# Kernel tuning notes

Measured on AMD Instinct MI355X. Metric: run time of the kernel, lower is better.

## Reference

```python
import jax, jax.numpy as jnp
import numpy as np

DIM = 256
BATCH = 131072


def setup_inputs() -> dict:
    key = jax.random.key(0)
    kx, kl, ku = jax.random.split(key, 3)
    x = jax.random.normal(kx, (BATCH, DIM), dtype=jnp.float32)
    # l: unit lower-triangular (eye + strict lower random), as in __init__
    l = jnp.eye(DIM, dtype=jnp.float32) + jnp.tril(
        jax.random.normal(kl, (DIM, DIM), dtype=jnp.float32), -1)
    # u: unit upper-triangular (eye + strict upper random)
    u = jnp.eye(DIM, dtype=jnp.float32) + jnp.triu(
        jax.random.normal(ku, (DIM, DIM), dtype=jnp.float32), 1)
    # p: fixed random permutation matrix (buffer, not trained)
    perm = np.random.RandomState(0).permutation(DIM)
    p = jnp.zeros((DIM, DIM), dtype=jnp.float32).at[
        np.arange(DIM), perm].set(1.0)
    return {"x": x, "p": p, "l": l, "u": u}


def reference(x, p, l, u):
    # forward (reverse=False): w = p @ l @ u ; y = (w @ x.T).T = x @ w.T
    w = p @ l @ u                      # [dim, dim]
    y = x @ w.T                        # [batch, dim]
    # log|det(w)| = log|det(u)| since p is a permutation (|det|=1) and l is
    # unit-triangular; u is upper-triangular so det(u) = prod(diag(u)).
    log_det = jnp.sum(jnp.log(jnp.abs(jnp.diag(u))))
    return (y, log_det)
```

## Files before the change

### kernel.cpp

```cpp
#include <hip/hip_runtime.h>

#define DIM 256
#define BATCH 131072

#define BM 128
#define BN 256
#define BK 32
#define STRIDE 40

typedef __attribute__((ext_vector_type(8))) short s16x8;
typedef __attribute__((ext_vector_type(8))) unsigned short u16x8;
typedef __attribute__((ext_vector_type(4))) float f32x4;

static __device__ __forceinline__ unsigned short f2bf(float f) {
    unsigned int u = __builtin_bit_cast(unsigned int, f);
    u = (u + 0x7FFFu + ((u >> 16) & 1u)) >> 16;
    return (unsigned short)u;
}

__global__ void lu_mm(const float* __restrict__ l, const float* __restrict__ u,
                      float* __restrict__ m) {
    __shared__ float sL[DIM];
    const int i = blockIdx.x, j = threadIdx.x;
    sL[j] = l[i * DIM + j];
    __syncthreads();
    float s0 = 0.f, s1 = 0.f, s2 = 0.f, s3 = 0.f;
    #pragma unroll 4
    for (int k = 0; k < DIM; k += 4) {
        s0 = fmaf(sL[k + 0], u[(k + 0) * DIM + j], s0);
        s1 = fmaf(sL[k + 1], u[(k + 1) * DIM + j], s1);
        s2 = fmaf(sL[k + 2], u[(k + 2) * DIM + j], s2);
        s3 = fmaf(sL[k + 3], u[(k + 3) * DIM + j], s3);
    }
    m[i * DIM + j] = (s0 + s1) + (s2 + s3);
}

__global__ void perm_conv(const float* __restrict__ p, const float* __restrict__ m,
                          unsigned short* __restrict__ wbt) {
    __shared__ int srcRow;
    const int i = blockIdx.x, j = threadIdx.x;
    if (p[i * DIM + j] != 0.0f) srcRow = j;
    __syncthreads();
    wbt[i * DIM + j] = f2bf(m[srcRow * DIM + j]);
}

__global__ void logdet_kernel(const float* __restrict__ u, float* __restrict__ out) {
    const int i = threadIdx.x;
    float v = logf(fabsf(u[i * DIM + i]));
    #pragma unroll
    for (int o = 32; o; o >>= 1) v += __shfl_down(v, o, 64);
    __shared__ float partial[4];
    if ((i & 63) == 0) partial[i >> 6] = v;
    __syncthreads();
    if (i == 0) out[0] = (partial[0] + partial[1]) + (partial[2] + partial[3]);
}

__global__ __launch_bounds__(512) void gemm_xwT(const float* __restrict__ x,
                                                const unsigned short* __restrict__ wbt,
                                                float* __restrict__ y) {
    __shared__ unsigned short sA[BM * STRIDE];
    __shared__ unsigned short sB[BN * STRIDE];

    const int t    = threadIdx.x;
    const int lane = t & 63;
    const int wid  = t >> 6;
    const int wr   = wid >> 2;
    const int wc   = wid & 3;
    const int row0 = blockIdx.x * BM;

    const int ar = t >> 2;
    const int ac = (t & 3) * 4;
    const int br = t >> 1;
    const int bc = (t & 1) * 16;

    const int lr = lane & 15;
    const int lg = lane >> 4;

    f32x4 acc[4][4];
    #pragma unroll
    for (int m = 0; m < 4; m++)
        #pragma unroll
        for (int n = 0; n < 4; n++) acc[m][n] = (f32x4){0.f, 0.f, 0.f, 0.f};

    for (int ks = 0; ks < DIM / BK; ++ks) {
        const int k0 = ks * BK;
        if (ks) __syncthreads();
        {
            const float* src = x + (size_t)(row0 + ar) * DIM + k0 + ac;
            const float4 v0 = *(const float4*)(src);
            const float4 v1 = *(const float4*)(src + 16);
            ushort4 h0 = { f2bf(v0.x), f2bf(v0.y), f2bf(v0.z), f2bf(v0.w) };
            ushort4 h1 = { f2bf(v1.x), f2bf(v1.y), f2bf(v1.z), f2bf(v1.w) };
            *(ushort4*)&sA[ar * STRIDE + ac]      = h0;
            *(ushort4*)&sA[ar * STRIDE + ac + 16] = h1;
        }
        {
            const unsigned short* src = wbt + br * DIM + k0 + bc;
            const u16x8 w0 = *(const u16x8*)(src);
            const u16x8 w1 = *(const u16x8*)(src + 8);
            *(u16x8*)&sB[br * STRIDE + bc]     = w0;
            *(u16x8*)&sB[br * STRIDE + bc + 8] = w1;
        }
        __syncthreads();

        s16x8 af[4], bfr[4];
        #pragma unroll
        for (int m = 0; m < 4; m++)
            af[m] = *(const s16x8*)&sA[(wr * 64 + m * 16 + lr) * STRIDE + lg * 8];
        #pragma unroll
        for (int n = 0; n < 4; n++)
            bfr[n] = *(const s16x8*)&sB[(wc * 64 + n * 16 + lr) * STRIDE + lg * 8];
        #pragma unroll
        for (int m = 0; m < 4; m++)
            #pragma unroll
            for (int n = 0; n < 4; n++)
                acc[m][n] = __builtin_amdgcn_mfma_f32_16x16x32_bf16(af[m], bfr[n], acc[m][n], 0, 0, 0);
    }

    #pragma unroll
    for (int m = 0; m < 4; m++) {
        const int gr0 = row0 + wr * 64 + m * 16 + lg * 4;
        #pragma unroll
        for (int n = 0; n < 4; n++) {
            const int gc = wc * 64 + n * 16 + lr;
            #pragma unroll
            for (int j = 0; j < 4; j++)
                y[(size_t)(gr0 + j) * DIM + gc] = acc[m][n][j];
        }
    }
}

extern "C" void kernel_launch(void* const* d_in, const int* in_sizes, int n_in,
                              void* d_out, int out_size, void* d_ws, size_t ws_size,
                              hipStream_t stream) {
    const float* x = (const float*)d_in[0];
    const float* p = (const float*)d_in[1];
    const float* l = (const float*)d_in[2];
    const float* u = (const float*)d_in[3];
    float* out = (float*)d_out;

    float* mtmp = (float*)d_ws;
    unsigned short* wbt = (unsigned short*)((char*)d_ws + DIM * DIM * 4);

    lu_mm<<<DIM, DIM, 0, stream>>>(l, u, mtmp);
    perm_conv<<<DIM, DIM, 0, stream>>>(p, mtmp, wbt);
    logdet_kernel<<<1, DIM, 0, stream>>>(u, out + (size_t)BATCH * DIM);
    gemm_xwT<<<BATCH / BM, 512, 0, stream>>>(x, wbt, out);
}
```

Baseline: 68.39 us.

## Drop LDS staging in GEMM, load MFMA fragments from global; fuse LU and permute

The GEMM no longer stages tiles in shared memory. Each wave loads its A fragments straight from global x, converting them to bf16 in registers, and its B fragments straight from the bf16 weight, with no __syncthreads. The block tile shrinks to 64 rows with launch bounds (512,4), which should raise occupancy. Separately, the L·U product and the permutation/bf16 conversion are fused into one kernel that scatters rows to their permuted destinations. This saves one launch and the intermediate buffer. The risks are less coalesced global access and redundant W reads per wave, which lean on the cache.

```diff
diff --git a/kernel.cpp b/kernel.cpp
--- a/kernel.cpp
+++ b/kernel.cpp
@@ -2,11 +2,8 @@
 
 #define DIM 256
 #define BATCH 131072
-
-#define BM 128
-#define BN 256
-#define BK 32
-#define STRIDE 40
+#define BM 64
+#define NT 8
 
 typedef __attribute__((ext_vector_type(8))) short s16x8;
 typedef __attribute__((ext_vector_type(8))) unsigned short u16x8;
@@ -18,11 +15,13 @@
     return (unsigned short)u;
 }
 
-__global__ void lu_mm(const float* __restrict__ l, const float* __restrict__ u,
-                      float* __restrict__ m) {
+__global__ void lu_perm(const float* __restrict__ l, const float* __restrict__ u,
+                        const float* __restrict__ p, unsigned short* __restrict__ wbt) {
     __shared__ float sL[DIM];
+    __shared__ int dest;
     const int i = blockIdx.x, j = threadIdx.x;
     sL[j] = l[i * DIM + j];
+    if (p[j * DIM + i] != 0.0f) dest = j;
     __syncthreads();
     float s0 = 0.f, s1 = 0.f, s2 = 0.f, s3 = 0.f;
     #pragma unroll 4
@@ -32,16 +31,7 @@
         s2 = fmaf(sL[k + 2], u[(k + 2) * DIM + j], s2);
         s3 = fmaf(sL[k + 3], u[(k + 3) * DIM + j], s3);
     }
-    m[i * DIM + j] = (s0 + s1) + (s2 + s3);
-}
-
-__global__ void perm_conv(const float* __restrict__ p, const float* __restrict__ m,
-                          unsigned short* __restrict__ wbt) {
-    __shared__ int srcRow;
-    const int i = blockIdx.x, j = threadIdx.x;
-    if (p[i * DIM + j] != 0.0f) srcRow = j;
-    __syncthreads();
-    wbt[i * DIM + j] = f2bf(m[srcRow * DIM + j]);
+    wbt[dest * DIM + j] = f2bf((s0 + s1) + (s2 + s3));
 }
 
 __global__ void logdet_kernel(const float* __restrict__ u, float* __restrict__ out) {
@@ -55,77 +45,63 @@
     if (i == 0) out[0] = (partial[0] + partial[1]) + (partial[2] + partial[3]);
 }
 
-__global__ __launch_bounds__(512) void gemm_xwT(const float* __restrict__ x,
-                                                const unsigned short* __restrict__ wbt,
-                                                float* __restrict__ y) {
-    __shared__ unsigned short sA[BM * STRIDE];
-    __shared__ unsigned short sB[BN * STRIDE];
-
+__global__ __launch_bounds__(512, 4) void gemm_xwT(const float* __restrict__ x,
+                                                   const unsigned short* __restrict__ wbt,
+                                                   float* __restrict__ y) {
     const int t    = threadIdx.x;
     const int lane = t & 63;
     const int wid  = t >> 6;
     const int wr   = wid >> 2;
     const int wc   = wid & 3;
-    const int row0 = blockIdx.x * BM;
+    const int lr   = lane & 15;
+    const int lg   = lane >> 4;
+    const long row0 = (long)blockIdx.x * BM;
 
-    const int ar = t >> 2;
-    const int ac = (t & 3) * 4;
-    const int br = t >> 1;
-    const int bc = (t & 1) * 16;
+    const float*          xa = x   + (row0 + wr * 32 + lr) * DIM + lg * 8;
+    const unsigned short* bb = wbt + (wc * 64 + lr) * DIM + lg * 8;
 
-    const int lr = lane & 15;
-    const int lg = lane >> 4;
-
-    f32x4 acc[4][4];
+    f32x4 acc[2][4];
     #pragma unroll
-    for (int m = 0; m < 4; m++)
+    for (int m = 0; m < 2; m++)
         #pragma unroll
         for (int n = 0; n < 4; n++) acc[m][n] = (f32x4){0.f, 0.f, 0.f, 0.f};
 
-    for (int ks = 0; ks < DIM / BK; ++ks) {
-        const int k0 = ks * BK;
-        if (ks) __syncthreads();
-        {
-            const float* src = x + (size_t)(row0 + ar) * DIM + k0 + ac;
-            const float4 v0 = *(const float4*)(src);
-            const float4 v1 = *(const float4*)(src + 16);
-            ushort4 h0 = { f2bf(v0.x), f2bf(v0.y), f2bf(v0.z), f2bf(v0.w) };
-            ushort4 h1 = { f2bf(v1.x), f2bf(v1.y), f2bf(v1.z), f2bf(v1.w) };
-            *(ushort4*)&sA[ar * STRIDE + ac]      = h0;
-            *(ushort4*)&sA[ar * STRIDE + ac + 16] = h1;
+    #pragma unroll
+    for (int ks = 0; ks < NT; ++ks) {
+        const int k0 = ks * 32;
+        s16x8 af[2];
+        s16x8 bfr[4];
+        #pragma unroll
+        for (int m = 0; m < 2; m++) {
+            const float* srcp = xa + (long)m * 16 * DIM + k0;
+            const float4 v0 = *(const float4*)(srcp);
+            const float4 v1 = *(const float4*)(srcp + 4);
+            af[m] = (s16x8){ (short)f2bf(v0.x), (short)f2bf(v0.y),
+                             (short)f2bf(v0.z), (short)f2bf(v0.w),
+                             (short)f2bf(v1.x), (short)f2bf(v1.y),
+                             (short)f2bf(v1.z), (short)f2bf(v1.w) };
         }
-        {
-            const unsigned short* src = wbt + br * DIM + k0 + bc;
-            const u16x8 w0 = *(const u16x8*)(src);
-            const u16x8 w1 = *(const u16x8*)(src + 8);
-            *(u16x8*)&sB[br * STRIDE + bc]     = w0;
-            *(u16x8*)&sB[br * STRIDE + bc + 8] = w1;
+        #pragma unroll
+        for (int n = 0; n < 4; n++) {
+            const u16x8 w = *(const u16x8*)(bb + n * 16 * DIM + k0);
+            bfr[n] = __builtin_bit_cast(s16x8, w);
         }
-        __syncthreads();
-
-        s16x8 af[4], bfr[4];
         #pragma unroll
-        for (int m = 0; m < 4; m++)
-            af[m] = *(const s16x8*)&sA[(wr * 64 + m * 16 + lr) * STRIDE + lg * 8];
-        #pragma unroll
-        for (int n = 0; n < 4; n++)
-            bfr[n] = *(const s16x8*)&sB[(wc * 64 + n * 16 + lr) * STRIDE + lg * 8];
-        #pragma unroll
-        for (int m = 0; m < 4; m++)
+        for (int m = 0; m < 2; m++)
             #pragma unroll
             for (int n = 0; n < 4; n++)
                 acc[m][n] = __builtin_amdgcn_mfma_f32_16x16x32_bf16(af[m], bfr[n], acc[m][n], 0, 0, 0);
     }
 
     #pragma unroll
-    for (int m = 0; m < 4; m++) {
-        const int gr0 = row0 + wr * 64 + m * 16 + lg * 4;
+    for (int m = 0; m < 2; m++) {
+        const long gr0 = row0 + wr * 32 + m * 16 + lg * 4;
         #pragma unroll
         for (int n = 0; n < 4; n++) {
             const int gc = wc * 64 + n * 16 + lr;
             #pragma unroll
             for (int j = 0; j < 4; j++)
-                y[(size_t)(gr0 + j) * DIM + gc] = acc[m][n][j];
+                y[(gr0 + j) * DIM + gc] = acc[m][n][j];
         }
     }
 }
@@ -139,11 +115,9 @@
     const float* u = (const float*)d_in[3];
     float* out = (float*)d_out;
 
-    float* mtmp = (float*)d_ws;
-    unsigned short* wbt = (unsigned short*)((char*)d_ws + DIM * DIM * 4);
+    unsigned short* wbt = (unsigned short*)d_ws;
 
-    lu_mm<<<DIM, DIM, 0, stream>>>(l, u, mtmp);
-    perm_conv<<<DIM, DIM, 0, stream>>>(p, mtmp, wbt);
+    lu_perm<<<DIM, DIM, 0, stream>>>(l, u, p, wbt);
     logdet_kernel<<<1, DIM, 0, stream>>>(u, out + (size_t)BATCH * DIM);
     gemm_xwT<<<BATCH / BM, 512, 0, stream>>>(x, wbt, out);
 }
```

New measurement: 141.8 us. 2.07x slower.
